# Kernel tuning notes

Measured on AMD Instinct MI355X. Metric: run time of the kernel, lower is better.

The kernel has to match this reference:

```python
import jax, jax.numpy as jnp
import numpy as np

D_MODEL = 1024
NUM_HEADS = 16
D_HEAD = D_MODEL // NUM_HEADS  # 64
LAMBDA_INIT = 0.8
EPS = 1e-5


def setup_inputs() -> dict:
    key = jax.random.key(0)
    ks = jax.random.split(key, 10)
    B, N = 2, 2048
    # Xavier-uniform-ish scale for the projection weights
    def xav(k, shape):
        fan_in, fan_out = shape[0], shape[1]
        lim = np.sqrt(6.0 / (fan_in + fan_out))
        return jax.random.uniform(k, shape, jnp.float32, -lim, lim)
    return {
        "X": jax.random.normal(ks[0], (B, N, D_MODEL), jnp.float32),
        "Wq": xav(ks[1], (D_MODEL, 2 * D_MODEL)),
        "Wk": xav(ks[2], (D_MODEL, 2 * D_MODEL)),
        "Wv": xav(ks[3], (D_MODEL, 2 * D_MODEL)),
        "Wo": xav(ks[4], (2 * D_MODEL, D_MODEL)),
        "lambda_q1": jax.random.normal(ks[5], (NUM_HEADS, D_HEAD), jnp.float32),
        "lambda_k1": jax.random.normal(ks[6], (NUM_HEADS, D_HEAD), jnp.float32),
        "lambda_q2": jax.random.normal(ks[7], (NUM_HEADS, D_HEAD), jnp.float32),
        "lambda_k2": jax.random.normal(ks[8], (NUM_HEADS, D_HEAD), jnp.float32),
        "rms_scale": jnp.ones((2 * D_HEAD,), jnp.float32),
    }


def reference(X, Wq, Wk, Wv, Wo, lambda_q1, lambda_k1, lambda_q2, lambda_k2, rms_scale):
    B, N, _ = X.shape
    H, Dh = NUM_HEADS, D_HEAD
    # projections -> [B, H, N, 2*Dh]
    Q = (X @ Wq).reshape(B, N, H, 2 * Dh).transpose(0, 2, 1, 3)
    K = (X @ Wk).reshape(B, N, H, 2 * Dh).transpose(0, 2, 1, 3)
    V = (X @ Wv).reshape(B, N, H, 2 * Dh).transpose(0, 2, 1, 3)
    Q1, Q2 = Q[..., :Dh], Q[..., Dh:]
    K1, K2 = K[..., :Dh], K[..., Dh:]
    # learned lambda per head
    lam = (jnp.exp(jnp.sum(lambda_q1 * lambda_k1, -1))
           - jnp.exp(jnp.sum(lambda_q2 * lambda_k2, -1))
           + LAMBDA_INIT)  # [H]
    scaling = 1.0 / np.sqrt(Dh)
    causal = jnp.tril(jnp.ones((N, N), bool))  # [N, N]
    neg_inf = jnp.float32(-jnp.inf)
    A1 = jnp.einsum('bhqd,bhkd->bhqk', Q1, K1) * scaling
    A2 = jnp.einsum('bhqd,bhkd->bhqk', Q2, K2) * scaling
    A1 = jnp.where(causal, A1, neg_inf)
    A2 = jnp.where(causal, A2, neg_inf)
    attn = jax.nn.softmax(A1, axis=-1) - lam[None, :, None, None] * jax.nn.softmax(A2, axis=-1)
    O = jnp.einsum('bhqk,bhkd->bhqd', attn, V)  # [B, H, N, 2*Dh]
    # per-(batch,head,pos) RMSNorm over the 2*Dh channel dim
    rms = jnp.sqrt(jnp.mean(O * O, axis=-1, keepdims=True) + EPS)
    O = O / rms * rms_scale
    O = O * (1.0 - LAMBDA_INIT)
    O = O.transpose(0, 2, 1, 3).reshape(B, N, H * 2 * Dh)
    return O @ Wo
```

## Files before the change

kernel.cpp:

```cpp
#include <hip/hip_runtime.h>
#include <hip/hip_bf16.h>

#define DM   1024
#define NH   16
#define DH   64
#define NSEQ 2048
#define NBATCH 2
#define ROWS (NBATCH*NSEQ)
#define QKVN (2*DM)
#define STR3 (3*DM*2)

typedef __attribute__((ext_vector_type(8))) short short8;
typedef __attribute__((ext_vector_type(4))) float f32x4;
typedef __attribute__((ext_vector_type(4))) unsigned short u16x4;

__device__ __forceinline__ unsigned short f2bf(float x) {
  union { float f; unsigned u; } v; v.f = x;
  unsigned r = v.u + 0x7FFFu + ((v.u >> 16) & 1u);
  return (unsigned short)(r >> 16);
}

__device__ __forceinline__ float exp2a(float x) {
  float r; asm("v_exp_f32 %0, %1" : "=v"(r) : "v"(x)); return r;
}
__device__ __forceinline__ unsigned cvtpk(float lo, float hi) {
  unsigned d; asm("v_cvt_pk_bf16_f32 %0, %1, %2" : "=v"(d) : "v"(lo), "v"(hi)); return d;
}

__device__ __forceinline__ f32x4 mfma16(short8 a, short8 b, f32x4 c) {
  return __builtin_amdgcn_mfma_f32_16x16x32_bf16(a, b, c, 0, 0, 0);
}

#define GLL(src, dst) \
  __builtin_amdgcn_global_load_lds((const __attribute__((address_space(1))) void*)(src), \
                                   (__attribute__((address_space(3))) void*)(dst), 16, 0, 0)

__global__ void prep_fused(const float* __restrict__ X,
                           const float* __restrict__ Wq, const float* __restrict__ Wk,
                           const float* __restrict__ Wv, const float* __restrict__ Wo,
                           unsigned short* __restrict__ Xb,
                           unsigned short* __restrict__ Wt,
                           unsigned short* __restrict__ Wot) {
  const int z = blockIdx.z;
  const int tx = threadIdx.x, ty = threadIdx.y;

  if (z == 4) {
    const int bid = blockIdx.y * 64 + blockIdx.x;
    const int t = ty * 32 + tx;
    #pragma unroll
    for (int j = 0; j < 2; ++j) {
      const int i = bid * 512 + j * 256 + t;
      f32x4 v = *(const f32x4*)(X + (size_t)i * 4);
      u16x4 o;
      #pragma unroll
      for (int k = 0; k < 4; ++k) o[k] = f2bf(v[k]);
      *(u16x4*)(Xb + (size_t)i * 4) = o;
    }
    return;
  }

  const float* in;
  unsigned short* out;
  int R, C, bx, by;
  if (z < 3) {
    in = (z == 0) ? Wq : (z == 1) ? Wk : Wv;
    out = Wt + (size_t)z * 2048 * 1024;
    R = DM; C = QKVN;
    bx = blockIdx.x; by = blockIdx.y;
  } else {
    in = Wo; out = Wot;
    R = QKVN; C = DM;
    bx = blockIdx.y; by = blockIdx.x;
  }

  __shared__ float tile[32][33];
  #pragma unroll
  for (int i = 0; i < 4; ++i)
    tile[ty + i*8][tx] = in[(size_t)(by*32 + ty + i*8) * C + bx*32 + tx];
  __syncthreads();
  #pragma unroll
  for (int i = 0; i < 4; ++i)
    out[(size_t)(bx*32 + ty + i*8) * R + by*32 + tx] = f2bf(tile[tx][ty + i*8]);
}

__global__ void transpose_v(const unsigned short* __restrict__ Vb, unsigned short* __restrict__ Vt) {
  __shared__ unsigned short tile[32][33];
  const int bx = blockIdx.x, by = blockIdx.y;
  const int tx = threadIdx.x, ty = threadIdx.y;
  #pragma unroll
  for (int i = 0; i < 4; ++i)
    tile[ty + i*8][tx] = Vb[(size_t)(by*32 + ty + i*8) * STR3 + bx*32 + tx];
  __syncthreads();
  #pragma unroll
  for (int i = 0; i < 4; ++i) {
    int colg = bx*32 + ty + i*8;
    int rowg = by*32 + tx;
    int hh = colg >> 7, dd = colg & 127;
    int bb = rowg >> 11, nn = rowg & 2047;
    Vt[(size_t)((bb*NH + hh)*128 + dd) * NSEQ + nn] = tile[tx][ty + i*8];
  }
}

__global__ void lam_kernel(const float* __restrict__ lq1, const float* __restrict__ lk1,
                           const float* __restrict__ lq2, const float* __restrict__ lk2,
                           float* __restrict__ lam) {
  int h = threadIdx.x >> 6, lane = threadIdx.x & 63;
  float p1 = lq1[h*64 + lane] * lk1[h*64 + lane];
  float p2 = lq2[h*64 + lane] * lk2[h*64 + lane];
  #pragma unroll
  for (int mk = 32; mk >= 1; mk >>= 1) {
    p1 += __shfl_xor(p1, mk);
    p2 += __shfl_xor(p2, mk);
  }
  if (lane == 0) lam[h] = expf(p1) - expf(p2) + 0.8f;
}

template <typename OT>
__global__ __launch_bounds__(256) void gemm_bt(const unsigned short* __restrict__ A,
                                               const unsigned short* __restrict__ Bt,
                                               OT* __restrict__ C, int M, int N, int K) {
  __shared__ __align__(16) unsigned short As[128*32];
  __shared__ __align__(16) unsigned short Bs[128*32];
  const int tid = threadIdx.x;
  const int w = tid >> 6, lane = tid & 63;
  const int l15 = lane & 15, lg = lane >> 4;
  const int wr = w >> 1, wc = w & 1;

  const unsigned gx = gridDim.x;
  unsigned bid = blockIdx.y * gx + blockIdx.x;
  const unsigned cpx = (gx * gridDim.y) >> 3;
  bid = (bid & 7u) * cpx + (bid >> 3);
  const int m0 = (int)(bid / gx) * 128, n0 = (int)(bid % gx) * 128;

  f32x4 acc[4][4];
  #pragma unroll
  for (int i = 0; i < 4; ++i)
    #pragma unroll
    for (int j = 0; j < 4; ++j) acc[i][j] = f32x4{0.f, 0.f, 0.f, 0.f};

  for (int kt = 0; kt < K; kt += 32) {
    #pragma unroll
    for (int j = 0; j < 2; ++j) {
      int cbase = (j*4 + w) * 64;
      int c = cbase + lane;
      const unsigned short* ga = A + (size_t)(m0 + (c >> 2)) * K + kt + (c & 3) * 8;
      GLL(ga, As + cbase*8);
      const unsigned short* gb = Bt + (size_t)(n0 + (c >> 2)) * K + kt + (c & 3) * 8;
      GLL(gb, Bs + cbase*8);
    }
    __syncthreads();
    short8 af[4], bfr[4];
    #pragma unroll
    for (int m = 0; m < 4; ++m)
      af[m] = *(const short8*)(As + (wr*64 + m*16 + l15) * 32 + lg*8);
    #pragma unroll
    for (int n = 0; n < 4; ++n)
      bfr[n] = *(const short8*)(Bs + (wc*64 + n*16 + l15) * 32 + lg*8);
    #pragma unroll
    for (int m = 0; m < 4; ++m)
      #pragma unroll
      for (int n = 0; n < 4; ++n)
        acc[m][n] = mfma16(af[m], bfr[n], acc[m][n]);
    __syncthreads();
  }

  #pragma unroll
  for (int m = 0; m < 4; ++m)
    #pragma unroll
    for (int n = 0; n < 4; ++n)
      #pragma unroll
      for (int r = 0; r < 4; ++r) {
        int row = m0 + wr*64 + m*16 + lg*4 + r;
        int col = n0 + wc*64 + n*16 + l15;
        if constexpr (sizeof(OT) == 2)
          C[(size_t)row * N + col] = f2bf(acc[m][n][r]);
        else
          C[(size_t)row * N + col] = acc[m][n][r];
      }
}

__global__ __launch_bounds__(256) void diff_attn(const unsigned short* __restrict__ QKV,
                                                 const unsigned short* __restrict__ Vt,
                                                 const float* __restrict__ lam_arr,
                                                 const float* __restrict__ rms_scale,
                                                 unsigned short* __restrict__ O) {
  __shared__ __align__(16) unsigned short Ks[2][64*128];
  __shared__ __align__(16) unsigned short Vs[2][128*64];
  __shared__ __align__(16) unsigned short Plds[4][2][16*64];

  const unsigned bid = blockIdx.x;
  const int xcd = (int)(bid & 7u), idx = (int)(bid >> 3);
  const int bh = xcd * 4 + (idx >> 4);
  const int jj = idx & 15;

  const int b = bh >> 4, h = bh & 15;
  const int w = threadIdx.x >> 6, lane = threadIdx.x & 63;
  const int l15 = lane & 15, lg = lane >> 4;
  const float lam = lam_arr[h];

  const unsigned short* Qb  = QKV + (size_t)(b * NSEQ) * STR3 + h * 128;
  const unsigned short* Kb  = QKV + (size_t)(b * NSEQ) * STR3 + 2048 + h * 128;
  const unsigned short* Vtb = Vt + (size_t)bh * 128 * NSEQ;

  auto stage = [&](int bufi, int key0) {
    #pragma unroll
    for (int j = 0; j < 4; ++j) {
      const int t = j*4 + w;
      {
        const int row = t*4 + (lane >> 4);
        const int ck  = lane & 15;
        const int cks = (ck & 8) | ((ck ^ row) & 7);
        GLL(Kb + (size_t)(key0 + row) * STR3 + cks*8, &Ks[bufi][t*512]);
      }
      {
        const int row = t*8 + (lane >> 3);
        const int ck  = lane & 7;
        const int cks = (ck ^ row) & 7;
        GLL(Vtb + (size_t)row * NSEQ + key0 + cks*8, &Vs[bufi][t*512]);
      }
    }
  };

  char* pb0 = (char*)&Plds[w][0][0];
  char* pb1 = (char*)&Plds[w][1][0];
  const unsigned swz = (unsigned)((l15 & 7) << 4);
  const float qsc = 0.125f * 1.44269504088896340736f;
  const int kx0 = ((lg ^ l15) & 7) * 8;
  const int kx1 = (((4 + lg) ^ l15) & 7) * 8;

  for (int pass = 0; pass < 2; ++pass) {
    const int qt = pass ? jj : 31 - jj;
    const int q0 = qt * 64 + w * 16;

    short8 a1[2], a2[2];
    #pragma unroll
    for (int kc = 0; kc < 2; ++kc) {
      const unsigned short* qp = Qb + (size_t)(q0 + l15) * STR3 + kc*32 + lg*8;
      short8 r1 = *(const short8*)qp;
      short8 r2 = *(const short8*)(qp + 64);
      #pragma unroll
      for (int j = 0; j < 8; j += 2) {
        union { unsigned u; float f; } x0, x1, y0, y1;
        x0.u = ((unsigned)(unsigned short)r1[j]) << 16;
        x1.u = ((unsigned)(unsigned short)r1[j+1]) << 16;
        y0.u = ((unsigned)(unsigned short)r2[j]) << 16;
        y1.u = ((unsigned)(unsigned short)r2[j+1]) << 16;
        unsigned d1 = cvtpk(x0.f * qsc, x1.f * qsc);
        unsigned d2 = cvtpk(y0.f * qsc, y1.f * qsc);
        a1[kc][j]   = (short)(unsigned short)(d1 & 0xffffu);
        a1[kc][j+1] = (short)(unsigned short)(d1 >> 16);
        a2[kc][j]   = (short)(unsigned short)(d2 & 0xffffu);
        a2[kc][j+1] = (short)(unsigned short)(d2 >> 16);
      }
    }

    f32x4 o1[8], o2[8];
    #pragma unroll
    for (int i = 0; i < 8; ++i) { o1[i] = f32x4{0,0,0,0}; o2[i] = f32x4{0,0,0,0}; }
    float m1 = -3e38f, l1 = 0.f, m2 = -3e38f, l2 = 0.f;

    stage(0, 0);
    __syncthreads();
    int buf = 0;

    for (int kb = 0; kb <= qt; ++kb) {
      const int key0 = kb * 64;
      if (kb < qt) stage(buf ^ 1, key0 + 64);

      f32x4 st1[4], st2[4];
      #pragma unroll
      for (int nb = 0; nb < 4; ++nb) { st1[nb] = f32x4{0,0,0,0}; st2[nb] = f32x4{0,0,0,0}; }
      __builtin_amdgcn_s_setprio(1);
      #pragma unroll
      for (int nb = 0; nb < 4; ++nb) {
        const unsigned short* krow = &Ks[buf][nb*2048 + l15*128];
        short8 k10 = *(const short8*)(krow + kx0);
        short8 k11 = *(const short8*)(krow + kx1);
        short8 k20 = *(const short8*)(krow + kx0 + 64);
        short8 k21 = *(const short8*)(krow + kx1 + 64);
        st1[nb] = mfma16(k10, a1[0], st1[nb]);
        st1[nb] = mfma16(k11, a1[1], st1[nb]);
        st2[nb] = mfma16(k20, a2[0], st2[nb]);
        st2[nb] = mfma16(k21, a2[1], st2[nb]);
      }
      __builtin_amdgcn_s_setprio(0);

      if (kb == qt) {
        #pragma unroll
        for (int nb = 0; nb < 4; ++nb)
          #pragma unroll
          for (int r = 0; r < 4; ++r)
            if (key0 + nb*16 + lg*4 + r > q0 + l15) { st1[nb][r] = -3e38f; st2[nb][r] = -3e38f; }
      }

      float tm1 = -3e38f, tm2 = -3e38f;
      #pragma unroll
      for (int nb = 0; nb < 4; ++nb)
        #pragma unroll
        for (int r = 0; r < 4; ++r) {
          tm1 = fmaxf(tm1, st1[nb][r]); tm2 = fmaxf(tm2, st2[nb][r]);
        }
      tm1 = fmaxf(tm1, __shfl_xor(tm1, 16));
      tm1 = fmaxf(tm1, __shfl_xor(tm1, 32));
      tm2 = fmaxf(tm2, __shfl_xor(tm2, 16));
      tm2 = fmaxf(tm2, __shfl_xor(tm2, 32));

      if (__any(tm1 > m1 + 8.f)) {
        const float nm = fmaxf(m1, tm1);
        const float e = exp2a(m1 - nm);
        m1 = nm; l1 *= e;
        float er[4];
        #pragma unroll
        for (int r = 0; r < 4; ++r) er[r] = __shfl(e, lg*4 + r);
        #pragma unroll
        for (int i = 0; i < 8; ++i)
          #pragma unroll
          for (int r = 0; r < 4; ++r) o1[i][r] *= er[r];
      }
      if (__any(tm2 > m2 + 8.f)) {
        const float nm = fmaxf(m2, tm2);
        const float e = exp2a(m2 - nm);
        m2 = nm; l2 *= e;
        float er[4];
        #pragma unroll
        for (int r = 0; r < 4; ++r) er[r] = __shfl(e, lg*4 + r);
        #pragma unroll
        for (int i = 0; i < 8; ++i)
          #pragma unroll
          for (int r = 0; r < 4; ++r) o2[i][r] *= er[r];
      }

      float ts1 = 0.f, ts2 = 0.f;
      #pragma unroll
      for (int nb = 0; nb < 4; ++nb)
        #pragma unroll
        for (int r = 0; r < 4; ++r) {
          st1[nb][r] = exp2a(st1[nb][r] - m1); ts1 += st1[nb][r];
          st2[nb][r] = exp2a(st2[nb][r] - m2); ts2 += st2[nb][r];
        }
      ts1 += __shfl_xor(ts1, 16); ts1 += __shfl_xor(ts1, 32); l1 += ts1;
      ts2 += __shfl_xor(ts2, 16); ts2 += __shfl_xor(ts2, 32); l2 += ts2;

      #pragma unroll
      for (int nb = 0; nb < 4; ++nb) {
        const unsigned off = (unsigned)(l15*128 + nb*32 + lg*8) ^ swz;
        *(uint2*)(pb0 + off) = make_uint2(cvtpk(st1[nb][0], st1[nb][1]),
                                          cvtpk(st1[nb][2], st1[nb][3]));
        *(uint2*)(pb1 + off) = make_uint2(cvtpk(st2[nb][0], st2[nb][1]),
                                          cvtpk(st2[nb][2], st2[nb][3]));
      }
      asm volatile("s_waitcnt lgkmcnt(0)" ::: "memory");
      __builtin_amdgcn_sched_barrier(0);
      short8 pa1[2], pa2[2];
      #pragma unroll
      for (int kc = 0; kc < 2; ++kc) {
        const unsigned off = (unsigned)(l15*128 + kc*64 + lg*16) ^ swz;
        pa1[kc] = *(const short8*)(pb0 + off);
        pa2[kc] = *(const short8*)(pb1 + off);
      }
      __builtin_amdgcn_sched_barrier(0);

      __builtin_amdgcn_s_setprio(1);
      #pragma unroll
      for (int i = 0; i < 8; ++i) {
        const unsigned short* vrow = &Vs[buf][(i*16 + l15) * 64];
        const short8 b0 = *(const short8*)(vrow + kx0);
        const short8 b1 = *(const short8*)(vrow + kx1);
        o1[i] = mfma16(pa1[0], b0, o1[i]);
        o2[i] = mfma16(pa2[0], b0, o2[i]);
        o1[i] = mfma16(pa1[1], b1, o1[i]);
        o2[i] = mfma16(pa2[1], b1, o2[i]);
      }
      __builtin_amdgcn_s_setprio(0);

      __syncthreads();
      buf ^= 1;
    }

    float i1r[4], i2r[4];
    {
      const float inv1 = 1.f / l1, inv2 = 1.f / l2;
      #pragma unroll
      for (int r = 0; r < 4; ++r) {
        i1r[r] = __shfl(inv1, lg*4 + r);
        i2r[r] = __shfl(inv2, lg*4 + r);
      }
    }
    float ov[8][4];
    float ssq[4] = {0.f, 0.f, 0.f, 0.f};
    #pragma unroll
    for (int i = 0; i < 8; ++i)
      #pragma unroll
      for (int r = 0; r < 4; ++r) {
        float v = o1[i][r] * i1r[r] - lam * (o2[i][r] * i2r[r]);
        ov[i][r] = v;
        ssq[r] += v * v;
      }
    #pragma unroll
    for (int r = 0; r < 4; ++r)
      #pragma unroll
      for (int mk = 1; mk < 16; mk <<= 1) ssq[r] += __shfl_xor(ssq[r], mk);
    float rr[4];
    #pragma unroll
    for (int r = 0; r < 4; ++r) rr[r] = rsqrtf(ssq[r] * (1.f/128.f) + 1e-5f) * 0.2f;
    #pragma unroll
    for (int i = 0; i < 8; ++i) {
      const float sc = rms_scale[i*16 + l15];
      #pragma unroll
      for (int r = 0; r < 4; ++r) {
        const int q = q0 + lg*4 + r;
        O[(size_t)(b*NSEQ + q) * QKVN + h*128 + i*16 + l15] = f2bf(ov[i][r] * rr[r] * sc);
      }
    }
  }
}

extern "C" void kernel_launch(void* const* d_in, const int* in_sizes, int n_in,
                              void* d_out, int out_size, void* d_ws, size_t ws_size,
                              hipStream_t stream) {
  (void)in_sizes; (void)n_in; (void)out_size; (void)ws_size;
  const float* X   = (const float*)d_in[0];
  const float* Wq  = (const float*)d_in[1];
  const float* Wk  = (const float*)d_in[2];
  const float* Wv  = (const float*)d_in[3];
  const float* Wo  = (const float*)d_in[4];
  const float* lq1 = (const float*)d_in[5];
  const float* lk1 = (const float*)d_in[6];
  const float* lq2 = (const float*)d_in[7];
  const float* lk2 = (const float*)d_in[8];
  const float* rs  = (const float*)d_in[9];
  float* out = (float*)d_out;

  char* ws = (char*)d_ws;
  const size_t MB = 1ull << 20;
  unsigned short* Xb  = (unsigned short*)(ws);
  unsigned short* Wt  = (unsigned short*)(ws + 8*MB);
  unsigned short* Wot = (unsigned short*)(ws + 20*MB);
  unsigned short* QKV = (unsigned short*)(ws + 24*MB);
  unsigned short* Ob  = (unsigned short*)(ws + 72*MB);
  float*          lamp = (float*)(ws + 88*MB);
  unsigned short* Vt  = (unsigned short*)(ws);

  prep_fused<<<dim3(64, 32, 5), dim3(32, 8), 0, stream>>>(X, Wq, Wk, Wv, Wo, Xb, Wt, Wot);
  lam_kernel<<<1, 1024, 0, stream>>>(lq1, lk1, lq2, lk2, lamp);

  gemm_bt<unsigned short><<<dim3(STR3/128, ROWS/128), 256, 0, stream>>>(Xb, Wt, QKV, ROWS, STR3, DM);

  transpose_v<<<dim3(QKVN/32, ROWS/32), dim3(32,8), 0, stream>>>(QKV + 4096, Vt);

  diff_attn<<<dim3(512), 256, 0, stream>>>(QKV, Vt, lamp, rs, Ob);

  gemm_bt<float><<<dim3(DM/128, ROWS/128), 256, 0, stream>>>(Ob, Wot, out, ROWS, DM, QKVN);
}
```

Measured before the change: 236.7 us.

## Replace QKV projection GEMM with 256x256 8-wave ping-pong pipelined kernel

Adds a new GEMM kernel for the QKV projection that uses 256x256 tiles, 512 threads and double-buffered LDS with swizzled layout. Direct global-to-LDS loads are interleaved between MFMA clusters, and barriers plus setprio are used to overlap memory with compute. The aim is higher arithmetic intensity and better latency hiding than the previous 128x128 kernel. Larger tiles give only 24x16=384 blocks and use heavy LDS and registers, which risks occupancy and tail effects.

```diff
diff --git a/kernel.cpp b/kernel.cpp
--- a/kernel.cpp
+++ b/kernel.cpp
@@ -34,6 +34,8 @@
 #define GLL(src, dst) \
   __builtin_amdgcn_global_load_lds((const __attribute__((address_space(1))) void*)(src), \
                                    (__attribute__((address_space(3))) void*)(dst), 16, 0, 0)
+
+#define WAITV(n) asm volatile("s_waitcnt vmcnt(" #n ")" ::: "memory")
 
 __global__ void prep_fused(const float* __restrict__ X,
                            const float* __restrict__ Wq, const float* __restrict__ Wk,
@@ -113,6 +115,147 @@
     p2 += __shfl_xor(p2, mk);
   }
   if (lane == 0) lam[h] = expf(p1) - expf(p2) + 0.8f;
+}
+
+template <typename OT>
+__global__ __launch_bounds__(512) void gemm8p(const unsigned short* __restrict__ A,
+                                              const unsigned short* __restrict__ Bt,
+                                              OT* __restrict__ C, int M, int N, int K, int ldc) {
+  __shared__ __align__(16) unsigned short As[2][2][256*32];
+  __shared__ __align__(16) unsigned short Bs[2][2][256*32];
+  (void)M; (void)N;
+  const int tid = threadIdx.x;
+  const int wv = tid >> 6, lane = tid & 63;
+  const int l15 = lane & 15, lg = lane >> 4;
+  const int wm = wv >> 2, wn = wv & 3;
+
+  const unsigned gx = gridDim.x;
+  unsigned bid = blockIdx.y * gx + blockIdx.x;
+  const unsigned cpx = (gx * gridDim.y) >> 3;
+  bid = (bid & 7u) * cpx + (bid >> 3);
+  const int m0 = (int)(bid / gx) * 256, n0 = (int)(bid % gx) * 256;
+
+  const int NT = K >> 6;
+
+  int rowS[2], subS[2];
+  #pragma unroll
+  for (int j = 0; j < 2; ++j) {
+    const int c = j*512 + tid;
+    rowS[j] = c >> 2;
+    const int s = c & 3;
+    subS[j] = (s ^ (rowS[j] & 3) ^ ((rowS[j] >> 2) & 3)) & 3;
+  }
+  const unsigned short* Ab = A  + (size_t)m0 * K;
+  const unsigned short* Bb = Bt + (size_t)n0 * K;
+
+  auto stA = [&](int b, int ks, int tt) {
+    #pragma unroll
+    for (int j = 0; j < 2; ++j)
+      GLL(Ab + (size_t)rowS[j]*K + tt*64 + ks*32 + subS[j]*8,
+          &As[b][ks][(j*512 + (wv << 6)) * 8]);
+  };
+  auto stB = [&](int b, int ks, int tt) {
+    #pragma unroll
+    for (int j = 0; j < 2; ++j)
+      GLL(Bb + (size_t)rowS[j]*K + tt*64 + ks*32 + subS[j]*8,
+          &Bs[b][ks][(j*512 + (wv << 6)) * 8]);
+  };
+
+  const int phys = ((lg ^ (l15 & 3) ^ ((l15 >> 2) & 3)) & 3) * 8;
+
+  auto rdA = [&](int b, int ks, int Mh, short8* af) {
+    #pragma unroll
+    for (int m = 0; m < 4; ++m) {
+      const int row = wm*128 + Mh*64 + m*16 + l15;
+      af[m] = *(const short8*)(&As[b][ks][row*32 + phys]);
+    }
+  };
+  auto rdB = [&](int b, int ks, short8* bf) {
+    #pragma unroll
+    for (int n = 0; n < 4; ++n) {
+      const int row = wn*64 + n*16 + l15;
+      bf[n] = *(const short8*)(&Bs[b][ks][row*32 + phys]);
+    }
+  };
+
+  f32x4 acc[8][4];
+  #pragma unroll
+  for (int i = 0; i < 8; ++i)
+    #pragma unroll
+    for (int j = 0; j < 4; ++j) acc[i][j] = f32x4{0.f, 0.f, 0.f, 0.f};
+
+  stA(0, 0, 0); stB(0, 0, 0); stA(0, 1, 0); stB(0, 1, 0);
+  stA(1, 0, 1); stB(1, 0, 1);
+  WAITV(4);
+  __builtin_amdgcn_s_barrier();
+
+  short8 af[4], bf[4];
+
+#define MFMA_CLUSTER(MH)                                               \
+    asm volatile("s_waitcnt lgkmcnt(0)" ::: "memory");                 \
+    __builtin_amdgcn_sched_barrier(0);                                 \
+    __builtin_amdgcn_s_setprio(1);                                     \
+    _Pragma("unroll")                                                  \
+    for (int m = 0; m < 4; ++m)                                        \
+      _Pragma("unroll")                                                \
+      for (int n = 0; n < 4; ++n)                                      \
+        acc[(MH)*4+m][n] = mfma16(af[m], bf[n], acc[(MH)*4+m][n]);     \
+    __builtin_amdgcn_s_setprio(0);                                     \
+    __builtin_amdgcn_s_barrier();
+
+  for (int t = 0; t < NT; t += 2) {
+    const bool s2 = (t + 2 < NT);
+    const bool s3 = (t + 3 < NT);
+
+    rdA(0, 0, 0, af); rdB(0, 0, bf);
+    stA(1, 1, t + 1);
+    __builtin_amdgcn_s_barrier();
+    MFMA_CLUSTER(0)
+    rdA(0, 0, 1, af);
+    stB(1, 1, t + 1);
+    __builtin_amdgcn_s_barrier();
+    MFMA_CLUSTER(1)
+    rdA(0, 1, 0, af); rdB(0, 1, bf);
+    if (s2) stA(0, 0, t + 2);
+    __builtin_amdgcn_s_barrier();
+    MFMA_CLUSTER(0)
+    rdA(0, 1, 1, af);
+    if (s2) { stB(0, 0, t + 2); WAITV(4); } else { WAITV(0); }
+    __builtin_amdgcn_s_barrier();
+    MFMA_CLUSTER(1)
+    rdA(1, 0, 0, af); rdB(1, 0, bf);
+    if (s2) stA(0, 1, t + 2);
+    __builtin_amdgcn_s_barrier();
+    MFMA_CLUSTER(0)
+    rdA(1, 0, 1, af);
+    if (s2) stB(0, 1, t + 2);
+    __builtin_amdgcn_s_barrier();
+    MFMA_CLUSTER(1)
+    rdA(1, 1, 0, af); rdB(1, 1, bf);
+    if (s3) stA(1, 0, t + 3);
+    __builtin_amdgcn_s_barrier();
+    MFMA_CLUSTER(0)
+    rdA(1, 1, 1, af);
+    if (s3) stB(1, 0, t + 3);
+    WAITV(4);
+    __builtin_amdgcn_s_barrier();
+    MFMA_CLUSTER(1)
+  }
+#undef MFMA_CLUSTER
+
+  #pragma unroll
+  for (int mi = 0; mi < 8; ++mi)
+    #pragma unroll
+    for (int n = 0; n < 4; ++n)
+      #pragma unroll
+      for (int r = 0; r < 4; ++r) {
+        const int row = m0 + wm*128 + (mi >> 2)*64 + (mi & 3)*16 + lg*4 + r;
+        const int col = n0 + wn*64 + n*16 + l15;
+        if constexpr (sizeof(OT) == 2)
+          C[(size_t)row * ldc + col] = f2bf(acc[mi][n][r]);
+        else
+          C[(size_t)row * ldc + col] = acc[mi][n][r];
+      }
 }
 
 template <typename OT>
@@ -444,7 +587,8 @@
   prep_fused<<<dim3(64, 32, 5), dim3(32, 8), 0, stream>>>(X, Wq, Wk, Wv, Wo, Xb, Wt, Wot);
   lam_kernel<<<1, 1024, 0, stream>>>(lq1, lk1, lq2, lk2, lamp);
 
-  gemm_bt<unsigned short><<<dim3(STR3/128, ROWS/128), 256, 0, stream>>>(Xb, Wt, QKV, ROWS, STR3, DM);
+  gemm8p<unsigned short><<<dim3(STR3/256, ROWS/256), 512, 0, stream>>>(
+      Xb, Wt, QKV, ROWS, STR3, DM, STR3);
 
   transpose_v<<<dim3(QKVN/32, ROWS/32), dim3(32,8), 0, stream>>>(QKV + 4096, Vt);
 
```

Result: no change. 236.7 us (-0.0%).
